# Performance work log

Hardware: AMD Instinct MI355X
Metric: run time of the kernel (lower is better)

The kernel has to match this reference:

```python
import jax, jax.numpy as jnp
import numpy as np

B, T, D_IN, H, E = 256, 512, 256, 256, 96  # batch, enc seq, input_size, hidden_size, num_embeddings


def setup_inputs() -> dict:
    key = jax.random.key(0)
    ks = jax.random.split(key, 12)
    s = 0.05
    return {
        "prev_h": jax.random.normal(ks[0], (B, H), jnp.float32),
        "prev_c": jax.random.normal(ks[1], (B, H), jnp.float32),
        "batch_H": jax.random.normal(ks[2], (B, T, D_IN), jnp.float32),
        "char_onehots": jax.random.uniform(ks[3], (B, E), jnp.float32),
        "W_i2h": jax.random.normal(ks[4], (H, D_IN), jnp.float32) * s,
        "W_h2h": jax.random.normal(ks[5], (H, H), jnp.float32) * s,
        "b_h2h": jax.random.normal(ks[6], (H,), jnp.float32) * s,
        "W_score": jax.random.normal(ks[7], (1, H), jnp.float32) * s,
        "W_ih": jax.random.normal(ks[8], (4 * H, D_IN + E), jnp.float32) * s,
        "W_hh": jax.random.normal(ks[9], (4 * H, H), jnp.float32) * s,
        "b_ih": jax.random.normal(ks[10], (4 * H,), jnp.float32) * s,
        "b_hh": jax.random.normal(ks[11], (4 * H,), jnp.float32) * s,
    }


def reference(prev_h, prev_c, batch_H, char_onehots,
              W_i2h, W_h2h, b_h2h, W_score, W_ih, W_hh, b_ih, b_hh):
    # additive attention over encoder features
    proj = jnp.einsum('btd,hd->bth', batch_H, W_i2h)          # [B,T,H]
    hid = prev_h @ W_h2h.T + b_h2h                             # [B,H]
    e = jnp.einsum('bth,oh->bto', jnp.tanh(proj + hid[:, None, :]), W_score)  # [B,T,1]
    alpha = jax.nn.softmax(e, axis=1)                          # [B,T,1]
    context = jnp.einsum('bt,btd->bd', alpha[..., 0], batch_H) # [B,D_IN]
    x = jnp.concatenate([context, char_onehots], axis=1)       # [B,D_IN+E]
    # LSTM cell step (PyTorch gate order: i, f, g, o)
    gates = x @ W_ih.T + b_ih + prev_h @ W_hh.T + b_hh         # [B,4H]
    i, f, g, o = jnp.split(gates, 4, axis=1)
    c_new = jax.nn.sigmoid(f) * prev_c + jax.nn.sigmoid(i) * jnp.tanh(g)
    h_new = jax.nn.sigmoid(o) * jnp.tanh(c_new)
    return (h_new, c_new, jnp.swapaxes(alpha, 1, 2))           # alpha -> [B,1,T]
```

## Files before the change

kernel.cpp:

```cpp
#include <hip/hip_runtime.h>

typedef __attribute__((ext_vector_type(8))) short short8;
typedef __attribute__((ext_vector_type(4))) float f32x4;

#define KPAD 40

#define WS_HID 0u
#define WS_CTX 262144u
#define WS_WBF 524288u

__device__ __forceinline__ unsigned cvtpk(float lo, float hi) {
    unsigned r;
    asm("v_cvt_pk_bf16_f32 %0, %1, %2" : "=v"(r) : "v"(lo), "v"(hi));
    return r;
}
__device__ __forceinline__ int4 pack8(float4 x0, float4 x1) {
    int4 q;
    q.x = (int)cvtpk(x0.x, x0.y);
    q.y = (int)cvtpk(x0.z, x0.w);
    q.z = (int)cvtpk(x1.x, x1.y);
    q.w = (int)cvtpk(x1.z, x1.w);
    return q;
}
__device__ __forceinline__ float bf2f(unsigned s) {
    union { float f; unsigned u; } v; v.u = s << 16;
    return v.f;
}
__device__ __forceinline__ float tanh_fast(float x) {
    float e2 = __expf(2.f * x);
    return 1.f - 2.f * __builtin_amdgcn_rcpf(e2 + 1.f);
}
__device__ __forceinline__ float sigmoid_fast(float x) {
    return __builtin_amdgcn_rcpf(1.f + __expf(-x));
}
__device__ __forceinline__ void gload16(const void* g, void* l) {
    __builtin_amdgcn_global_load_lds((const __attribute__((address_space(1))) void*)g,
                                     (__attribute__((address_space(3))) void*)l, 16, 0, 0);
}

__global__ __launch_bounds__(256) void k_prep(
    const float* __restrict__ prev_h, const float* __restrict__ W_i2h,
    const float* __restrict__ W_h2h, const float* __restrict__ b_h2h,
    float* __restrict__ hid, int4* __restrict__ Wbf)
{
    int bid = blockIdx.x, tid = threadIdx.x;
    if (bid < 256) {
        __shared__ float ph[256];
        ph[tid] = prev_h[bid * 256 + tid];
        __syncthreads();
        float acc = b_h2h[tid];
        const float4* w = (const float4*)(W_h2h + tid * 256);
        #pragma unroll 8
        for (int k4 = 0; k4 < 64; ++k4) {
            float4 ww = w[k4];
            acc += ww.x * ph[k4*4+0] + ww.y * ph[k4*4+1] + ww.z * ph[k4*4+2] + ww.w * ph[k4*4+3];
        }
        hid[bid * 256 + tid] = acc;
    } else {
        int u = (bid - 256) * 256 + tid;
        int cf = u >> 9, ks = (u >> 6) & 7;
        int n = cf * 16 + (u & 15);
        int k0 = ks * 32 + ((u >> 4) & 3) * 8;
        float4 x0 = *(const float4*)(W_i2h + n * 256 + k0);
        float4 x1 = *(const float4*)(W_i2h + n * 256 + k0 + 4);
        Wbf[u] = pack8(x0, x1);
    }
}

__global__ __launch_bounds__(512, 2) void k_attn(
    const float* __restrict__ BH, const int4* __restrict__ Wbf,
    const float* __restrict__ hid, const float* __restrict__ Wsc,
    float* __restrict__ alpha, float* __restrict__ ctx)
{
    __shared__ short Blds[65536];
    __shared__ float hdl[256], wscl[256];
    __shared__ float pl8[8][16];
    __shared__ float pls[32][16];
    __shared__ float r8[8][256];
    __shared__ float zsh[8];

    const int tid = threadIdx.x;
    const int lane = tid & 63;
    const int w8 = tid >> 6;
    const int l15 = lane & 15, lg = lane >> 4;
    const int b = blockIdx.x;

    int4 la[16];
    #define ISSUE_A(tile_)                                                          \
        {                                                                           \
            const float* base_ = BH + ((size_t)b * 512 + (tile_) * 16 + l15) * 256  \
                                 + lg * 8;                                          \
            asm volatile(                                                           \
                "global_load_dwordx4 %0, %16, off offset:0\n"                       \
                "global_load_dwordx4 %1, %16, off offset:16\n"                      \
                "global_load_dwordx4 %2, %16, off offset:128\n"                     \
                "global_load_dwordx4 %3, %16, off offset:144\n"                     \
                "global_load_dwordx4 %4, %16, off offset:256\n"                     \
                "global_load_dwordx4 %5, %16, off offset:272\n"                     \
                "global_load_dwordx4 %6, %16, off offset:384\n"                     \
                "global_load_dwordx4 %7, %16, off offset:400\n"                     \
                "global_load_dwordx4 %8, %16, off offset:512\n"                     \
                "global_load_dwordx4 %9, %16, off offset:528\n"                     \
                "global_load_dwordx4 %10, %16, off offset:640\n"                    \
                "global_load_dwordx4 %11, %16, off offset:656\n"                    \
                "global_load_dwordx4 %12, %16, off offset:768\n"                    \
                "global_load_dwordx4 %13, %16, off offset:784\n"                    \
                "global_load_dwordx4 %14, %16, off offset:896\n"                    \
                "global_load_dwordx4 %15, %16, off offset:912\n"                    \
                : "=v"(la[0]), "=v"(la[1]), "=v"(la[2]), "=v"(la[3]),               \
                  "=v"(la[4]), "=v"(la[5]), "=v"(la[6]), "=v"(la[7]),               \
                  "=v"(la[8]), "=v"(la[9]), "=v"(la[10]), "=v"(la[11]),             \
                  "=v"(la[12]), "=v"(la[13]), "=v"(la[14]), "=v"(la[15])            \
                : "v"(base_));                                                      \
        }

    ISSUE_A(w8);

    {
        const char* g = (const char*)Wbf;
        #pragma unroll
        for (int rnd = 0; rnd < 16; ++rnd)
            gload16(g + rnd * 8192 + tid * 16, (char*)Blds + rnd * 8192 + tid * 16);
    }
    if (tid < 256) { hdl[tid] = hid[b * 256 + tid]; wscl[tid] = Wsc[tid]; }
    ((float4*)r8)[tid] = (float4){0.f, 0.f, 0.f, 0.f};
    __syncthreads();

    float zacc = 0.f;

    #pragma unroll
    for (int ti = 0; ti < 4; ++ti) {
        const int tile = ti * 8 + w8;
        asm volatile("s_waitcnt vmcnt(0)" ::: "memory");
        __builtin_amdgcn_sched_barrier(0);
        short8 af[8];
        #pragma unroll
        for (int ks = 0; ks < 8; ++ks) {
            float4 f0, f1;
            *(int4*)&f0 = la[2 * ks];
            *(int4*)&f1 = la[2 * ks + 1];
            *(int4*)&af[ks] = pack8(f0, f1);
        }
        if (ti < 3) ISSUE_A(tile + 8);

        float esum[4] = {0.f, 0.f, 0.f, 0.f};
        #pragma unroll
        for (int h2 = 0; h2 < 2; ++h2) {
            f32x4 acc[8];
            #pragma unroll
            for (int c = 0; c < 8; ++c) acc[c] = (f32x4){0.f, 0.f, 0.f, 0.f};
            #pragma unroll
            for (int ks = 0; ks < 8; ++ks)
                #pragma unroll
                for (int c = 0; c < 8; ++c)
                    acc[c] = __builtin_amdgcn_mfma_f32_16x16x32_bf16(af[ks],
                        *(const short8*)&Blds[(((h2 * 8 + c) * 512) + ks * 64 + lane) * 8],
                        acc[c], 0, 0, 0);
            #pragma unroll
            for (int c = 0; c < 8; ++c) {
                int col = (h2 * 8 + c) * 16 + l15;
                float wv = wscl[col], hv = hdl[col];
                #pragma unroll
                for (int r = 0; r < 4; ++r)
                    esum[r] += wv * tanh_fast(acc[c][r] + hv);
            }
        }
        #pragma unroll
        for (int r = 0; r < 4; ++r) {
            float s = esum[r];
            s += __shfl_xor(s, 1); s += __shfl_xor(s, 2);
            s += __shfl_xor(s, 4); s += __shfl_xor(s, 8);
            esum[r] = s;
        }
        float ps = 0.f;
        #pragma unroll
        for (int r = 0; r < 4; ++r) {
            float pr = __expf(esum[r]);
            ps += pr;
            esum[r] = pr;
        }
        ps += __shfl_xor(ps, 16); ps += __shfl_xor(ps, 32);
        zacc += ps;
        if (l15 == 0) {
            #pragma unroll
            for (int r = 0; r < 4; ++r) {
                pl8[w8][lg * 4 + r] = esum[r];
                pls[tile][lg * 4 + r] = esum[r];
            }
        }
        float pv = pl8[w8][l15];
        #pragma unroll
        for (int ks = 0; ks < 8; ++ks) {
            float v[8];
            #pragma unroll
            for (int j = 0; j < 8; ++j) {
                v[j] = pv * bf2f((unsigned)(unsigned short)af[ks][j]);
                v[j] += __shfl_xor(v[j], 1); v[j] += __shfl_xor(v[j], 2);
                v[j] += __shfl_xor(v[j], 4); v[j] += __shfl_xor(v[j], 8);
            }
            if (l15 == 0) {
                #pragma unroll
                for (int j = 0; j < 8; ++j)
                    r8[w8][ks * 32 + lg * 8 + j] += v[j];
            }
        }
    }

    if (lane == 0) zsh[w8] = zacc;
    __syncthreads();
    float Z = 0.f;
    #pragma unroll
    for (int i = 0; i < 8; ++i) Z += zsh[i];
    const float inv = 1.f / Z;
    if (tid < 256) {
        alpha[b * 512 + tid]       = pls[tid >> 4][tid & 15] * inv;
        alpha[b * 512 + 256 + tid] = pls[16 + (tid >> 4)][tid & 15] * inv;
        float s = 0.f;
        #pragma unroll
        for (int ww = 0; ww < 8; ++ww) s += r8[ww][tid];
        ctx[b * 256 + tid] = s * inv;
    }
    #undef ISSUE_A
}

__global__ __launch_bounds__(256) void k_gates_lstm(
    const float* __restrict__ ctx, const float* __restrict__ onehot,
    const float* __restrict__ prev_h, const float* __restrict__ W_ih,
    const float* __restrict__ W_hh, const float* __restrict__ b_ih,
    const float* __restrict__ b_hh, const float* __restrict__ prev_c,
    float* __restrict__ out)
{
    __shared__ char smem[20800];
    short* AlB = (short*)smem;
    short* BlB = (short*)smem + 5120;
    const int tid = threadIdx.x;
    const int lane = tid & 63;
    const int w = tid >> 6;
    const int l15 = lane & 15, lg = lane >> 4;
    const int rb = blockIdx.x * 64;
    const int hb = blockIdx.y;

    f32x4 acc[4];
    #pragma unroll
    for (int j = 0; j < 4; j++) acc[j] = (f32x4){0.f, 0.f, 0.f, 0.f};

    const int arow = tid >> 2, akg = tid & 3;
    const int rg = rb + arow;
    const int bn = tid >> 2, bq = tid & 3;
    const int np_ = hb * 64 + bn, hh_ = np_ >> 2, gg_ = np_ & 3;
    const float* wih_row = W_ih + (size_t)(gg_ * 256 + hh_) * 352;
    const float* whh_row = W_hh + (size_t)(gg_ * 256 + hh_) * 256;

    auto stageAB = [&](int kc, int bu) {
        int k0 = kc * 32 + akg * 8;
        const float4* pa;
        if (k0 < 256)      pa = (const float4*)(ctx    + rg * 256 + k0);
        else if (k0 < 352) pa = (const float4*)(onehot + rg * 96  + (k0 - 256));
        else               pa = (const float4*)(prev_h + rg * 256 + (k0 - 352));
        float4 x0 = pa[0], x1 = pa[1];
        *(int4*)&AlB[bu * 2560 + arow * KPAD + akg * 8] = pack8(x0, x1);
        int kb = kc * 32 + bq * 8;
        const float* pb = (kb < 352) ? (wih_row + kb) : (whh_row + (kb - 352));
        float4 y0 = *(const float4*)pb, y1 = *(const float4*)(pb + 4);
        *(int4*)&BlB[bu * 2560 + bn * KPAD + bq * 8] = pack8(y0, y1);
    };

    stageAB(0, 0);
    __syncthreads();

    for (int kc = 0; kc < 19; ++kc) {
        int cur = kc & 1;
        short8 af = *(const short8*)&AlB[cur * 2560 + (w * 16 + l15) * KPAD + lg * 8];
        short8 bfr[4];
        #pragma unroll
        for (int cf = 0; cf < 4; cf++)
            bfr[cf] = *(const short8*)&BlB[cur * 2560 + (cf * 16 + l15) * KPAD + lg * 8];
        if (kc < 18) stageAB(kc + 1, cur ^ 1);
        #pragma unroll
        for (int cf = 0; cf < 4; cf++)
            acc[cf] = __builtin_amdgcn_mfma_f32_16x16x32_bf16(af, bfr[cf], acc[cf], 0, 0, 0);
        __syncthreads();
    }

    float* Gt = (float*)smem;
    #pragma unroll
    for (int cf = 0; cf < 4; cf++) {
        int col = cf * 16 + l15;
        int np = hb * 64 + col;
        int hg = np >> 2, g = np & 3;
        float bias = b_ih[g * 256 + hg] + b_hh[g * 256 + hg];
        #pragma unroll
        for (int r = 0; r < 4; r++)
            Gt[(w * 16 + lg * 4 + r) * 65 + col] = acc[cf][r] + bias;
    }
    __syncthreads();

    #pragma unroll
    for (int it = 0; it < 4; ++it) {
        int elem = it * 256 + tid;
        int row = elem >> 4, hl = elem & 15;
        float gi = Gt[row * 65 + hl * 4 + 0];
        float gf = Gt[row * 65 + hl * 4 + 1];
        float gg = Gt[row * 65 + hl * 4 + 2];
        float go = Gt[row * 65 + hl * 4 + 3];
        int bg = rb + row, hglob = hb * 16 + hl;
        float cv = sigmoid_fast(gf) * prev_c[bg * 256 + hglob] + sigmoid_fast(gi) * tanh_fast(gg);
        out[bg * 256 + hglob] = sigmoid_fast(go) * tanh_fast(cv);
        out[65536 + bg * 256 + hglob] = cv;
    }
}

extern "C" void kernel_launch(void* const* d_in, const int* in_sizes, int n_in,
                              void* d_out, int out_size, void* d_ws, size_t ws_size,
                              hipStream_t stream) {
    (void)in_sizes; (void)n_in; (void)out_size; (void)ws_size;
    const float* prev_h  = (const float*)d_in[0];
    const float* prev_c  = (const float*)d_in[1];
    const float* batch_H = (const float*)d_in[2];
    const float* onehot  = (const float*)d_in[3];
    const float* W_i2h   = (const float*)d_in[4];
    const float* W_h2h   = (const float*)d_in[5];
    const float* b_h2h   = (const float*)d_in[6];
    const float* W_score = (const float*)d_in[7];
    const float* W_ih    = (const float*)d_in[8];
    const float* W_hh    = (const float*)d_in[9];
    const float* b_ih    = (const float*)d_in[10];
    const float* b_hh    = (const float*)d_in[11];

    char* ws = (char*)d_ws;
    float* hid = (float*)(ws + WS_HID);
    float* ctx = (float*)(ws + WS_CTX);
    int4*  Wbf = (int4*)(ws + WS_WBF);

    float* out = (float*)d_out;
    float* alpha = out + 131072;

    hipLaunchKernelGGL(k_prep,       dim3(288),   dim3(256), 0, stream,
                       prev_h, W_i2h, W_h2h, b_h2h, hid, Wbf);
    hipLaunchKernelGGL(k_attn,       dim3(256),   dim3(512), 0, stream,
                       batch_H, Wbf, hid, W_score, alpha, ctx);
    hipLaunchKernelGGL(k_gates_lstm, dim3(4, 16), dim3(256), 0, stream,
                       ctx, onehot, prev_h, W_ih, W_hh, b_ih, b_hh, prev_c, out);
}
```

Before: 79.54 us.

## Double-buffer activation loads and compute context via second pass over batch_H

The attention kernel now keeps two register buffers of encoder rows in flight, prefetching two tiles ahead with partial vmcnt waits instead of waiting on all loads each iteration. The per-tile shuffle-reduction for the context vector is removed. Context is instead computed after the softmax by a coalesced re-read of batch_H (likely served from L2) weighted by the stored probabilities. Occupancy is lowered to one block per CU to make room for the extra registers. This trades a second global read of batch_H, and lower occupancy, for fewer shuffles and better load latency hiding.

```diff
diff --git a/kernel.cpp b/kernel.cpp
--- a/kernel.cpp
+++ b/kernel.cpp
@@ -21,10 +21,6 @@
     q.z = (int)cvtpk(x1.x, x1.y);
     q.w = (int)cvtpk(x1.z, x1.w);
     return q;
-}
-__device__ __forceinline__ float bf2f(unsigned s) {
-    union { float f; unsigned u; } v; v.u = s << 16;
-    return v.f;
 }
 __device__ __forceinline__ float tanh_fast(float x) {
     float e2 = __expf(2.f * x);
@@ -67,16 +63,15 @@
     }
 }
 
-__global__ __launch_bounds__(512, 2) void k_attn(
+__global__ __launch_bounds__(512, 1) void k_attn(
     const float* __restrict__ BH, const int4* __restrict__ Wbf,
     const float* __restrict__ hid, const float* __restrict__ Wsc,
     float* __restrict__ alpha, float* __restrict__ ctx)
 {
     __shared__ short Blds[65536];
     __shared__ float hdl[256], wscl[256];
-    __shared__ float pl8[8][16];
-    __shared__ float pls[32][16];
-    __shared__ float r8[8][256];
+    __shared__ float pls[512];
+    __shared__ float r2[2][256];
     __shared__ float zsh[8];
 
     const int tid = threadIdx.x;
@@ -85,8 +80,8 @@
     const int l15 = lane & 15, lg = lane >> 4;
     const int b = blockIdx.x;
 
-    int4 la[16];
-    #define ISSUE_A(tile_)                                                          \
+    int4 la0[16], la1[16];
+    #define ISSUE_A(LA, tile_)                                                      \
         {                                                                           \
             const float* base_ = BH + ((size_t)b * 512 + (tile_) * 16 + l15) * 256  \
                                  + lg * 8;                                          \
@@ -107,14 +102,15 @@
                 "global_load_dwordx4 %13, %16, off offset:784\n"                    \
                 "global_load_dwordx4 %14, %16, off offset:896\n"                    \
                 "global_load_dwordx4 %15, %16, off offset:912\n"                    \
-                : "=v"(la[0]), "=v"(la[1]), "=v"(la[2]), "=v"(la[3]),               \
-                  "=v"(la[4]), "=v"(la[5]), "=v"(la[6]), "=v"(la[7]),               \
-                  "=v"(la[8]), "=v"(la[9]), "=v"(la[10]), "=v"(la[11]),             \
-                  "=v"(la[12]), "=v"(la[13]), "=v"(la[14]), "=v"(la[15])            \
+                : "=v"(LA[0]), "=v"(LA[1]), "=v"(LA[2]), "=v"(LA[3]),               \
+                  "=v"(LA[4]), "=v"(LA[5]), "=v"(LA[6]), "=v"(LA[7]),               \
+                  "=v"(LA[8]), "=v"(LA[9]), "=v"(LA[10]), "=v"(LA[11]),             \
+                  "=v"(LA[12]), "=v"(LA[13]), "=v"(LA[14]), "=v"(LA[15])            \
                 : "v"(base_));                                                      \
         }
 
-    ISSUE_A(w8);
+    ISSUE_A(la0, w8);
+    ISSUE_A(la1, w8 + 8);
 
     {
         const char* g = (const char*)Wbf;
@@ -123,7 +119,6 @@
             gload16(g + rnd * 8192 + tid * 16, (char*)Blds + rnd * 8192 + tid * 16);
     }
     if (tid < 256) { hdl[tid] = hid[b * 256 + tid]; wscl[tid] = Wsc[tid]; }
-    ((float4*)r8)[tid] = (float4){0.f, 0.f, 0.f, 0.f};
     __syncthreads();
 
     float zacc = 0.f;
@@ -131,17 +126,18 @@
     #pragma unroll
     for (int ti = 0; ti < 4; ++ti) {
         const int tile = ti * 8 + w8;
-        asm volatile("s_waitcnt vmcnt(0)" ::: "memory");
-        __builtin_amdgcn_sched_barrier(0);
+        if (ti == 2) { asm volatile("s_waitcnt vmcnt(16)" ::: "memory"); __builtin_amdgcn_sched_barrier(0); }
+        if (ti == 3) { asm volatile("s_waitcnt vmcnt(0)"  ::: "memory"); __builtin_amdgcn_sched_barrier(0); }
         short8 af[8];
         #pragma unroll
         for (int ks = 0; ks < 8; ++ks) {
             float4 f0, f1;
-            *(int4*)&f0 = la[2 * ks];
-            *(int4*)&f1 = la[2 * ks + 1];
+            if ((ti & 1) == 0) { *(int4*)&f0 = la0[2 * ks]; *(int4*)&f1 = la0[2 * ks + 1]; }
+            else               { *(int4*)&f0 = la1[2 * ks]; *(int4*)&f1 = la1[2 * ks + 1]; }
             *(int4*)&af[ks] = pack8(f0, f1);
         }
-        if (ti < 3) ISSUE_A(tile + 8);
+        if (ti == 0) ISSUE_A(la0, tile + 16);
+        if (ti == 1) ISSUE_A(la1, tile + 16);
 
         float esum[4] = {0.f, 0.f, 0.f, 0.f};
         #pragma unroll
@@ -183,42 +179,33 @@
         zacc += ps;
         if (l15 == 0) {
             #pragma unroll
-            for (int r = 0; r < 4; ++r) {
-                pl8[w8][lg * 4 + r] = esum[r];
-                pls[tile][lg * 4 + r] = esum[r];
-            }
-        }
-        float pv = pl8[w8][l15];
-        #pragma unroll
-        for (int ks = 0; ks < 8; ++ks) {
-            float v[8];
-            #pragma unroll
-            for (int j = 0; j < 8; ++j) {
-                v[j] = pv * bf2f((unsigned)(unsigned short)af[ks][j]);
-                v[j] += __shfl_xor(v[j], 1); v[j] += __shfl_xor(v[j], 2);
-                v[j] += __shfl_xor(v[j], 4); v[j] += __shfl_xor(v[j], 8);
-            }
-            if (l15 == 0) {
-                #pragma unroll
-                for (int j = 0; j < 8; ++j)
-                    r8[w8][ks * 32 + lg * 8 + j] += v[j];
-            }
+            for (int r = 0; r < 4; ++r)
+                pls[tile * 16 + lg * 4 + r] = esum[r];
         }
     }
 
     if (lane == 0) zsh[w8] = zacc;
     __syncthreads();
+
     float Z = 0.f;
     #pragma unroll
     for (int i = 0; i < 8; ++i) Z += zsh[i];
     const float inv = 1.f / Z;
+
+    {
+        const int d = tid & 255, rh = tid >> 8;
+        const float* bh = BH + ((size_t)b * 512 + rh * 256) * 256 + d;
+        const float* pp = &pls[rh * 256];
+        float acc = 0.f;
+        #pragma unroll 16
+        for (int tt = 0; tt < 256; ++tt) acc += pp[tt] * bh[(size_t)tt * 256];
+        r2[rh][d] = acc;
+    }
+    __syncthreads();
     if (tid < 256) {
-        alpha[b * 512 + tid]       = pls[tid >> 4][tid & 15] * inv;
-        alpha[b * 512 + 256 + tid] = pls[16 + (tid >> 4)][tid & 15] * inv;
-        float s = 0.f;
-        #pragma unroll
-        for (int ww = 0; ww < 8; ++ww) s += r8[ww][tid];
-        ctx[b * 256 + tid] = s * inv;
+        alpha[b * 512 + tid]       = pls[tid] * inv;
+        alpha[b * 512 + 256 + tid] = pls[256 + tid] * inv;
+        ctx[b * 256 + tid] = (r2[0][tid] + r2[1][tid]) * inv;
     }
     #undef ISSUE_A
 }
```

After: 86.54 us. 8.8% more time.

## Restructure attention kernel to 1024 threads with 32 rows per wave

Applied to the files above, without the earlier changes.

The attention kernel moves from 512 threads looping over four 16-row tiles per wave to 1024 threads where each wave loads its 32 rows of batch_H at once. Each B-fragment read from LDS now feeds two MFMAs, so LDS traffic per MFMA is halved, and the manually pipelined inline-asm prefetch is dropped in favour of a single up-front load. The weighted context partials are written once per wave instead of accumulated across tiles. The trade-offs are one block per CU using about 148KB of LDS, no overlap between global loads and compute within a block, and higher register pressure under the 1024-thread launch bound.

```diff
diff --git a/kernel.cpp b/kernel.cpp
--- a/kernel.cpp
+++ b/kernel.cpp
@@ -67,160 +67,140 @@
     }
 }
 
-__global__ __launch_bounds__(512, 2) void k_attn(
+__global__ __launch_bounds__(1024, 1) void k_attn(
     const float* __restrict__ BH, const int4* __restrict__ Wbf,
     const float* __restrict__ hid, const float* __restrict__ Wsc,
     float* __restrict__ alpha, float* __restrict__ ctx)
 {
-    __shared__ short Blds[65536];
-    __shared__ float hdl[256], wscl[256];
-    __shared__ float pl8[8][16];
-    __shared__ float pls[32][16];
-    __shared__ float r8[8][256];
-    __shared__ float zsh[8];
+    __shared__ char smem[151616];
+    short* Blds = (short*)smem;
+    float* r16  = (float*)(smem + 131072);
+    float* pls  = (float*)(smem + 147456);
+    float* hdl  = (float*)(smem + 149504);
+    float* wscl = (float*)(smem + 150528);
+    float* zsh  = (float*)(smem + 151552);
 
     const int tid = threadIdx.x;
     const int lane = tid & 63;
-    const int w8 = tid >> 6;
+    const int w16 = tid >> 6;
     const int l15 = lane & 15, lg = lane >> 4;
     const int b = blockIdx.x;
-
-    int4 la[16];
-    #define ISSUE_A(tile_)                                                          \
-        {                                                                           \
-            const float* base_ = BH + ((size_t)b * 512 + (tile_) * 16 + l15) * 256  \
-                                 + lg * 8;                                          \
-            asm volatile(                                                           \
-                "global_load_dwordx4 %0, %16, off offset:0\n"                       \
-                "global_load_dwordx4 %1, %16, off offset:16\n"                      \
-                "global_load_dwordx4 %2, %16, off offset:128\n"                     \
-                "global_load_dwordx4 %3, %16, off offset:144\n"                     \
-                "global_load_dwordx4 %4, %16, off offset:256\n"                     \
-                "global_load_dwordx4 %5, %16, off offset:272\n"                     \
-                "global_load_dwordx4 %6, %16, off offset:384\n"                     \
-                "global_load_dwordx4 %7, %16, off offset:400\n"                     \
-                "global_load_dwordx4 %8, %16, off offset:512\n"                     \
-                "global_load_dwordx4 %9, %16, off offset:528\n"                     \
-                "global_load_dwordx4 %10, %16, off offset:640\n"                    \
-                "global_load_dwordx4 %11, %16, off offset:656\n"                    \
-                "global_load_dwordx4 %12, %16, off offset:768\n"                    \
-                "global_load_dwordx4 %13, %16, off offset:784\n"                    \
-                "global_load_dwordx4 %14, %16, off offset:896\n"                    \
-                "global_load_dwordx4 %15, %16, off offset:912\n"                    \
-                : "=v"(la[0]), "=v"(la[1]), "=v"(la[2]), "=v"(la[3]),               \
-                  "=v"(la[4]), "=v"(la[5]), "=v"(la[6]), "=v"(la[7]),               \
-                  "=v"(la[8]), "=v"(la[9]), "=v"(la[10]), "=v"(la[11]),             \
-                  "=v"(la[12]), "=v"(la[13]), "=v"(la[14]), "=v"(la[15])            \
-                : "v"(base_));                                                      \
-        }
-
-    ISSUE_A(w8);
+    const int tr0 = w16 * 32;
 
     {
         const char* g = (const char*)Wbf;
         #pragma unroll
-        for (int rnd = 0; rnd < 16; ++rnd)
-            gload16(g + rnd * 8192 + tid * 16, (char*)Blds + rnd * 8192 + tid * 16);
+        for (int rnd = 0; rnd < 8; ++rnd)
+            gload16(g + rnd * 16384 + tid * 16, (char*)Blds + rnd * 16384 + tid * 16);
     }
     if (tid < 256) { hdl[tid] = hid[b * 256 + tid]; wscl[tid] = Wsc[tid]; }
-    ((float4*)r8)[tid] = (float4){0.f, 0.f, 0.f, 0.f};
+
+    short8 af[2][8];
+    {
+        const float* base = BH + ((size_t)b * 512 + tr0 + l15) * 256 + lg * 8;
+        #pragma unroll
+        for (int rf = 0; rf < 2; ++rf)
+            #pragma unroll
+            for (int ks = 0; ks < 8; ++ks) {
+                const float* p4 = base + rf * 16 * 256 + ks * 32;
+                float4 x0 = *(const float4*)p4;
+                float4 x1 = *(const float4*)(p4 + 4);
+                *(int4*)&af[rf][ks] = pack8(x0, x1);
+            }
+    }
     __syncthreads();
 
-    float zacc = 0.f;
-
-    #pragma unroll
-    for (int ti = 0; ti < 4; ++ti) {
-        const int tile = ti * 8 + w8;
-        asm volatile("s_waitcnt vmcnt(0)" ::: "memory");
-        __builtin_amdgcn_sched_barrier(0);
-        short8 af[8];
-        #pragma unroll
-        for (int ks = 0; ks < 8; ++ks) {
-            float4 f0, f1;
-            *(int4*)&f0 = la[2 * ks];
-            *(int4*)&f1 = la[2 * ks + 1];
-            *(int4*)&af[ks] = pack8(f0, f1);
-        }
-        if (ti < 3) ISSUE_A(tile + 8);
-
-        float esum[4] = {0.f, 0.f, 0.f, 0.f};
-        #pragma unroll
-        for (int h2 = 0; h2 < 2; ++h2) {
-            f32x4 acc[8];
-            #pragma unroll
-            for (int c = 0; c < 8; ++c) acc[c] = (f32x4){0.f, 0.f, 0.f, 0.f};
-            #pragma unroll
-            for (int ks = 0; ks < 8; ++ks)
+    float esum[2][4];
+    #pragma unroll
+    for (int rf = 0; rf < 2; ++rf)
+        #pragma unroll
+        for (int r = 0; r < 4; ++r) esum[rf][r] = 0.f;
+
+    #pragma unroll
+    for (int cg = 0; cg < 4; ++cg) {
+        f32x4 acc[2][4];
+        #pragma unroll
+        for (int rf = 0; rf < 2; ++rf)
+            #pragma unroll
+            for (int c = 0; c < 4; ++c) acc[rf][c] = (f32x4){0.f, 0.f, 0.f, 0.f};
+        #pragma unroll
+        for (int ks = 0; ks < 8; ++ks)
+            #pragma unroll
+            for (int c = 0; c < 4; ++c) {
+                short8 bfr = *(const short8*)&Blds[(((cg * 4 + c) * 512) + ks * 64 + lane) * 8];
                 #pragma unroll
-                for (int c = 0; c < 8; ++c)
-                    acc[c] = __builtin_amdgcn_mfma_f32_16x16x32_bf16(af[ks],
-                        *(const short8*)&Blds[(((h2 * 8 + c) * 512) + ks * 64 + lane) * 8],
-                        acc[c], 0, 0, 0);
-            #pragma unroll
-            for (int c = 0; c < 8; ++c) {
-                int col = (h2 * 8 + c) * 16 + l15;
-                float wv = wscl[col], hv = hdl[col];
+                for (int rf = 0; rf < 2; ++rf)
+                    acc[rf][c] = __builtin_amdgcn_mfma_f32_16x16x32_bf16(af[rf][ks], bfr, acc[rf][c], 0, 0, 0);
+            }
+        #pragma unroll
+        for (int c = 0; c < 4; ++c) {
+            int col = (cg * 4 + c) * 16 + l15;
+            float wv = wscl[col], hv = hdl[col];
+            #pragma unroll
+            for (int rf = 0; rf < 2; ++rf)
                 #pragma unroll
                 for (int r = 0; r < 4; ++r)
-                    esum[r] += wv * tanh_fast(acc[c][r] + hv);
-            }
+                    esum[rf][r] += wv * tanh_fast(acc[rf][c][r] + hv);
         }
+    }
+
+    float zacc = 0.f;
+    #pragma unroll
+    for (int rf = 0; rf < 2; ++rf)
         #pragma unroll
         for (int r = 0; r < 4; ++r) {
-            float s = esum[r];
+            float s = esum[rf][r];
             s += __shfl_xor(s, 1); s += __shfl_xor(s, 2);
             s += __shfl_xor(s, 4); s += __shfl_xor(s, 8);
-            esum[r] = s;
+            float pr = __expf(s);
+            esum[rf][r] = pr;
+            zacc += pr;
         }
-        float ps = 0.f;
-        #pragma unroll
-        for (int r = 0; r < 4; ++r) {
-            float pr = __expf(esum[r]);
-            ps += pr;
-            esum[r] = pr;
-        }
-        ps += __shfl_xor(ps, 16); ps += __shfl_xor(ps, 32);
-        zacc += ps;
-        if (l15 == 0) {
-            #pragma unroll
-            for (int r = 0; r < 4; ++r) {
-                pl8[w8][lg * 4 + r] = esum[r];
-                pls[tile][lg * 4 + r] = esum[r];
-            }
-        }
-        float pv = pl8[w8][l15];
+    zacc += __shfl_xor(zacc, 16); zacc += __shfl_xor(zacc, 32);
+    if (l15 == 0) {
+        #pragma unroll
+        for (int rf = 0; rf < 2; ++rf)
+            #pragma unroll
+            for (int r = 0; r < 4; ++r)
+                pls[tr0 + rf * 16 + lg * 4 + r] = esum[rf][r];
+    }
+    if (lane == 0) zsh[w16] = zacc;
+
+    {
+        float pv0 = pls[tr0 + l15];
+        float pv1 = pls[tr0 + 16 + l15];
         #pragma unroll
         for (int ks = 0; ks < 8; ++ks) {
             float v[8];
             #pragma unroll
             for (int j = 0; j < 8; ++j) {
-                v[j] = pv * bf2f((unsigned)(unsigned short)af[ks][j]);
+                v[j] = pv0 * bf2f((unsigned)(unsigned short)af[0][ks][j])
+                     + pv1 * bf2f((unsigned)(unsigned short)af[1][ks][j]);
                 v[j] += __shfl_xor(v[j], 1); v[j] += __shfl_xor(v[j], 2);
                 v[j] += __shfl_xor(v[j], 4); v[j] += __shfl_xor(v[j], 8);
             }
             if (l15 == 0) {
                 #pragma unroll
                 for (int j = 0; j < 8; ++j)
-                    r8[w8][ks * 32 + lg * 8 + j] += v[j];
+                    r16[w16 * 256 + ks * 32 + lg * 8 + j] = v[j];
             }
         }
     }
-
-    if (lane == 0) zsh[w8] = zacc;
     __syncthreads();
+
     float Z = 0.f;
     #pragma unroll
-    for (int i = 0; i < 8; ++i) Z += zsh[i];
+    for (int i = 0; i < 16; ++i) Z += zsh[i];
     const float inv = 1.f / Z;
     if (tid < 256) {
-        alpha[b * 512 + tid]       = pls[tid >> 4][tid & 15] * inv;
-        alpha[b * 512 + 256 + tid] = pls[16 + (tid >> 4)][tid & 15] * inv;
         float s = 0.f;
         #pragma unroll
-        for (int ww = 0; ww < 8; ++ww) s += r8[ww][tid];
+        for (int ww = 0; ww < 16; ++ww) s += r16[ww * 256 + tid];
         ctx[b * 256 + tid] = s * inv;
-    }
-    #undef ISSUE_A
+    } else if (tid < 768) {
+        int i = tid - 256;
+        alpha[b * 512 + i] = pls[i] * inv;
+    }
 }
 
 __global__ __launch_bounds__(256) void k_gates_lstm(
@@ -335,10 +315,10 @@
     float* out = (float*)d_out;
     float* alpha = out + 131072;
 
-    hipLaunchKernelGGL(k_prep,       dim3(288),   dim3(256), 0, stream,
+    hipLaunchKernelGGL(k_prep,       dim3(288),   dim3(256),  0, stream,
                        prev_h, W_i2h, W_h2h, b_h2h, hid, Wbf);
-    hipLaunchKernelGGL(k_attn,       dim3(256),   dim3(512), 0, stream,
+    hipLaunchKernelGGL(k_attn,       dim3(256),   dim3(1024), 0, stream,
                        batch_H, Wbf, hid, W_score, alpha, ctx);
-    hipLaunchKernelGGL(k_gates_lstm, dim3(4, 16), dim3(256), 0, stream,
+    hipLaunchKernelGGL(k_gates_lstm, dim3(4, 16), dim3(256),  0, stream,
                        ctx, onehot, prev_h, W_ih, W_hh, b_ih, b_hh, prev_c, out);
 }
```

Result: no change. 80.74 us (+1.5%).
